# Optimization experiments

Measured on AMD Instinct MI355X. Metric: run time of the kernel, lower is better.

The kernel has to match this reference:

```python
import jax, jax.numpy as jnp
import numpy as np

R, CH, N, E, C, OUT, ED = 2, 2, 20000, 100000, 256, 256, 16


def setup_inputs() -> dict:
    key = jax.random.key(0)
    ks = jax.random.split(key, 11)
    inv = 1.0 / np.sqrt(C)
    return {
        "x": jax.random.normal(ks[0], (R * CH * N, C), jnp.float32),
        "edge_attr": jax.random.normal(ks[1], (E, ED), jnp.float32),
        "edge_weight": jax.random.uniform(ks[2], (R, CH, E, 1), jnp.float32),
        "lin_W": jax.random.normal(ks[3], (C, C), jnp.float32) * inv,
        "lin_b": jax.random.normal(ks[4], (C,), jnp.float32) * inv,
        "linl_W": jax.random.normal(ks[5], (C, OUT), jnp.float32) * inv,
        "linl_b": jax.random.normal(ks[6], (OUT,), jnp.float32) * inv,
        "linr_W": jax.random.normal(ks[7], (C, OUT), jnp.float32) * inv,
        "bond_W": jax.random.normal(ks[8], (ED, C), jnp.float32) / np.sqrt(ED),
        "bond_b": jax.random.normal(ks[9], (C,), jnp.float32) / np.sqrt(ED),
        "edge_index": jax.random.randint(ks[10], (2, E), 0, N, jnp.int64),
    }


def reference(x, edge_attr, edge_weight, lin_W, lin_b, linl_W, linl_b, linr_W,
              bond_W, bond_b, edge_index):
    # bond encoder: (E, ED) -> (E, C), broadcasts as (1, 1, E, C)
    edge_emb = edge_attr @ bond_W + bond_b
    x_l = x @ lin_W + lin_b                      # (R*CH*N, C)
    ux = x_l.reshape(R, CH, N, C)
    src = edge_index[0]
    dst = edge_index[1]
    # gather + add + GELU (exact/erf, matching torch F.gelu) + weight
    msg = jax.nn.gelu(ux[:, :, src, :] + edge_emb, approximate=False) * edge_weight  # (R,CH,E,C)
    # scatter_mean over edge targets
    sums = jnp.zeros((R, CH, N, C), x.dtype).at[:, :, dst, :].add(msg)
    cnt = jnp.zeros((N,), x.dtype).at[dst].add(1.0)
    out = sums / jnp.maximum(cnt, 1.0)[None, None, :, None]
    out = out.reshape(-1, C)                     # (R*CH*N, C)
    return out @ linl_W + linl_b + x @ linr_W
```

## Files before the change

kernel.cpp:

```cpp
#include <hip/hip_runtime.h>
#include <math.h>

#define NN 20000
#define EE 100000
#define CC 256
#define EDM 16
#define RC 4
#define MTOT (RC * NN)

typedef __attribute__((ext_vector_type(8))) short short8;
typedef __attribute__((ext_vector_type(4))) float floatx4;

#define LDK 72

__device__ __forceinline__ unsigned short f2bf(float f) {
    union { float f; unsigned u; } v; v.f = f;
    unsigned r = v.u + 0x7FFF + ((v.u >> 16) & 1);
    return (unsigned short)(r >> 16);
}
__device__ __forceinline__ float bf2f(unsigned short h) {
    union { unsigned u; float f; } v; v.u = ((unsigned)h) << 16;
    return v.f;
}

__device__ __forceinline__ float gelu_fast(float v) {
    const float ax = fabsf(v) * 0.70710678118654752f;
    const float t  = __builtin_amdgcn_rcpf(fmaf(0.3275911f, ax, 1.0f));
    const float p  = t * fmaf(t, fmaf(t, fmaf(t, fmaf(t, 1.061405429f,
                                -1.453152027f), 1.421413741f), -0.284496736f),
                              0.254829592f);
    const float e  = __builtin_amdgcn_exp2f(ax * ax * -1.4426950408889634f);
    const float erf_ax = fmaf(-p, e, 1.0f);
    return fmaf(0.5f * fabsf(v), erf_ax, 0.5f * v);
}

__global__ void k_prep_count(const float* __restrict__ lin_W,
                             const float* __restrict__ linl_W,
                             const float* __restrict__ linr_W,
                             unsigned short* __restrict__ linWT,
                             unsigned short* __restrict__ WbT,
                             const int* __restrict__ eidx,
                             int* __restrict__ cnt) {
    const int b = blockIdx.x;
    const int t = threadIdx.x;
    if (b < CC) {
        linWT[b * CC + t]      = f2bf(lin_W[t * CC + b]);
        WbT[b * 512 + t]       = f2bf(linl_W[t * CC + b]);
        WbT[b * 512 + 256 + t] = f2bf(linr_W[t * CC + b]);
    } else {
        int e = (b - CC) * 256 + t;
        if (e < EE) atomicAdd(cnt + eidx[EE + e], 1);
    }
}

template <int KTOT, int OUTBF16, int A1BF16>
__global__ __launch_bounds__(256) void k_mm(const float* __restrict__ A1f,
                                            const unsigned short* __restrict__ A1b,
                                            const float* __restrict__ A2,
                                            const unsigned short* __restrict__ BT,
                                            const float* __restrict__ bias,
                                            float* __restrict__ Cf,
                                            unsigned short* __restrict__ Cb) {
    __shared__ unsigned short As[64 * LDK];
    __shared__ unsigned short Bs[256 * LDK];
    const int tid  = threadIdx.x;
    const int lane = tid & 63;
    const int wave = tid >> 6;
    const int i0   = blockIdx.x * 64;
    const int l15  = lane & 15;
    const int q4   = lane >> 4;

    floatx4 acc[4][4];
#pragma unroll
    for (int mt = 0; mt < 4; mt++)
#pragma unroll
        for (int nt = 0; nt < 4; nt++) acc[mt][nt] = (floatx4)0.0f;

    for (int kc = 0; kc < KTOT; kc += 64) {
        __syncthreads();
        const int first = (kc < 256);
        const int kco   = first ? kc : kc - 256;
#pragma unroll
        for (int it = 0; it < 2; it++) {
            int q = tid + it * 256;
            int r = q >> 3;
            int c = q & 7;
            if (A1BF16 && first) {
                *(uint4*)(As + r * LDK + c * 8) =
                    *(const uint4*)(A1b + (size_t)(i0 + r) * CC + kco + c * 8);
            } else {
                const float* src = (first ? A1f : A2) + (size_t)(i0 + r) * CC + kco + c * 8;
                float4 v0 = *(const float4*)(src);
                float4 v1 = *(const float4*)(src + 4);
                uint4 p;
                p.x = (unsigned)f2bf(v0.x) | ((unsigned)f2bf(v0.y) << 16);
                p.y = (unsigned)f2bf(v0.z) | ((unsigned)f2bf(v0.w) << 16);
                p.z = (unsigned)f2bf(v1.x) | ((unsigned)f2bf(v1.y) << 16);
                p.w = (unsigned)f2bf(v1.z) | ((unsigned)f2bf(v1.w) << 16);
                *(uint4*)(As + r * LDK + c * 8) = p;
            }
        }
#pragma unroll
        for (int it = 0; it < 8; it++) {
            int q = tid + it * 256;
            int n = q >> 3;
            int c = q & 7;
            *(uint4*)(Bs + n * LDK + c * 8) =
                *(const uint4*)(BT + (size_t)n * KTOT + kc + c * 8);
        }
        __syncthreads();
#pragma unroll
        for (int kk = 0; kk < 64; kk += 32) {
            short8 a[4], b[4];
#pragma unroll
            for (int mt = 0; mt < 4; mt++)
                a[mt] = *(const short8*)(As + (mt * 16 + l15) * LDK + kk + q4 * 8);
#pragma unroll
            for (int nt = 0; nt < 4; nt++)
                b[nt] = *(const short8*)(Bs + (wave * 64 + nt * 16 + l15) * LDK + kk + q4 * 8);
#pragma unroll
            for (int mt = 0; mt < 4; mt++)
#pragma unroll
                for (int nt = 0; nt < 4; nt++)
                    acc[mt][nt] = __builtin_amdgcn_mfma_f32_16x16x32_bf16(
                        a[mt], b[nt], acc[mt][nt], 0, 0, 0);
        }
    }
#pragma unroll
    for (int nt = 0; nt < 4; nt++) {
        const int col = wave * 64 + nt * 16 + l15;
        const float bz = bias[col];
#pragma unroll
        for (int mt = 0; mt < 4; mt++) {
#pragma unroll
            for (int r = 0; r < 4; r++) {
                const int row = i0 + mt * 16 + q4 * 4 + r;
                const float v = acc[mt][nt][r] + bz;
                if (OUTBF16) Cb[(size_t)row * CC + col] = f2bf(v);
                else         Cf[(size_t)row * CC + col] = v;
            }
        }
    }
}

#define SCAN_T 1024
#define SCHUNK 20
__global__ __launch_bounds__(1024) void k_scan(const int* __restrict__ cnt,
                                               int* __restrict__ offs,
                                               int* __restrict__ cursor) {
    __shared__ int ps[SCAN_T];
    const int t = threadIdx.x;
    const int base = t * SCHUNK;
    int s = 0;
#pragma unroll
    for (int i = 0; i < SCHUNK; i++) {
        int idx = base + i;
        if (idx < NN) s += cnt[idx];
    }
    ps[t] = s;
    __syncthreads();
    for (int off = 1; off < SCAN_T; off <<= 1) {
        int v = (t >= off) ? ps[t - off] : 0;
        __syncthreads();
        ps[t] += v;
        __syncthreads();
    }
    int excl = (t == 0) ? 0 : ps[t - 1];
#pragma unroll
    for (int i = 0; i < SCHUNK; i++) {
        int idx = base + i;
        if (idx < NN) {
            offs[idx]   = excl;
            cursor[idx] = excl;
            excl += cnt[idx];
        }
    }
    if (t == SCAN_T - 1) offs[NN] = ps[SCAN_T - 1];
}

__global__ void k_scatter(const int* __restrict__ eidx, int* __restrict__ cursor,
                          int* __restrict__ bucket) {
    int e = blockIdx.x * 256 + threadIdx.x;
    if (e < EE) {
        int d = eidx[EE + e];
        int p = atomicAdd(cursor + d, 1);
        bucket[p] = e;
    }
}

template <int MEANBF16>
__global__ __launch_bounds__(256) void k_agg(const unsigned short* __restrict__ xlb,
                                             const float* __restrict__ edge_attr,
                                             const float* __restrict__ ew,
                                             const float* __restrict__ bond_W,
                                             const float* __restrict__ bond_b,
                                             const int* __restrict__ eidx,
                                             const int* __restrict__ offs,
                                             const int* __restrict__ bucket,
                                             float* __restrict__ mean_f,
                                             unsigned short* __restrict__ mean_b) {
    const int n = blockIdx.x;
    const int c = threadIdx.x;
    const int beg = offs[n], end = offs[n + 1];
    const float bb = bond_b[c];
    float bw[EDM];
#pragma unroll
    for (int k = 0; k < EDM; k++) bw[k] = bond_W[k * CC + c];

    float a0 = 0.f, a1 = 0.f, a2 = 0.f, a3 = 0.f;

#pragma unroll 2
    for (int j = beg; j < end; j++) {
        const int e   = __builtin_amdgcn_readfirstlane(bucket[j]);
        const int src = __builtin_amdgcn_readfirstlane(eidx[e]);
        const float w0 = ew[e];
        const float w1 = ew[EE + e];
        const float w2 = ew[2 * EE + e];
        const float w3 = ew[3 * EE + e];
        const float* ea = edge_attr + (size_t)e * EDM;
        float emb = bb;
#pragma unroll
        for (int k = 0; k < EDM; k++)
            emb = fmaf(ea[k], bw[k], emb);
        const size_t sb = (size_t)src * CC + c;
        float v0 = bf2f(xlb[sb])                       + emb;
        float v1 = bf2f(xlb[sb + (size_t)NN * CC])     + emb;
        float v2 = bf2f(xlb[sb + (size_t)2 * NN * CC]) + emb;
        float v3 = bf2f(xlb[sb + (size_t)3 * NN * CC]) + emb;
        a0 += gelu_fast(v0) * w0;
        a1 += gelu_fast(v1) * w1;
        a2 += gelu_fast(v2) * w2;
        a3 += gelu_fast(v3) * w3;
    }
    const float inv = 1.0f / fmaxf((float)(end - beg), 1.0f);
    const size_t ob = (size_t)n * CC + c;
    if (MEANBF16) {
        mean_b[ob]                       = f2bf(a0 * inv);
        mean_b[ob + (size_t)NN * CC]     = f2bf(a1 * inv);
        mean_b[ob + (size_t)2 * NN * CC] = f2bf(a2 * inv);
        mean_b[ob + (size_t)3 * NN * CC] = f2bf(a3 * inv);
    } else {
        mean_f[ob]                       = a0 * inv;
        mean_f[ob + (size_t)NN * CC]     = a1 * inv;
        mean_f[ob + (size_t)2 * NN * CC] = a2 * inv;
        mean_f[ob + (size_t)3 * NN * CC] = a3 * inv;
    }
}

extern "C" void kernel_launch(void* const* d_in, const int* in_sizes, int n_in,
                              void* d_out, int out_size, void* d_ws, size_t ws_size,
                              hipStream_t stream) {
    (void)in_sizes; (void)n_in; (void)out_size;
    const float* x           = (const float*)d_in[0];
    const float* edge_attr   = (const float*)d_in[1];
    const float* edge_weight = (const float*)d_in[2];
    const float* lin_W       = (const float*)d_in[3];
    const float* lin_b       = (const float*)d_in[4];
    const float* linl_W      = (const float*)d_in[5];
    const float* linl_b      = (const float*)d_in[6];
    const float* linr_W      = (const float*)d_in[7];
    const float* bond_W      = (const float*)d_in[8];
    const float* bond_b      = (const float*)d_in[9];
    const int*   edge_index  = (const int*)d_in[10];

    unsigned short* xlb   = (unsigned short*)d_ws;
    unsigned short* linWT = xlb + (size_t)MTOT * CC;
    unsigned short* WbT   = linWT + CC * CC;
    int* cnt    = (int*)(WbT + CC * 512);
    int* offs   = cnt + NN;
    int* cursor = offs + NN + 1;
    int* bucket = cursor + NN;
    uintptr_t mb_addr = (((uintptr_t)(bucket + EE)) + 255) & ~(uintptr_t)255;
    unsigned short* mean_b = (unsigned short*)mb_addr;
    const size_t need = (mb_addr - (uintptr_t)d_ws) + (size_t)MTOT * CC * 2;
    const int use_bf16 = (ws_size >= need);

    hipMemsetAsync(cnt, 0, NN * sizeof(int), stream);

    k_prep_count<<<CC + (EE + 255) / 256, 256, 0, stream>>>(
        lin_W, linl_W, linr_W, linWT, WbT, edge_index, cnt);
    k_mm<256, 1, 0><<<MTOT / 64, 256, 0, stream>>>(x, nullptr, x, linWT, lin_b,
                                                   nullptr, xlb);
    k_scan<<<1, SCAN_T, 0, stream>>>(cnt, offs, cursor);
    k_scatter<<<(EE + 255) / 256, 256, 0, stream>>>(edge_index, cursor, bucket);

    if (use_bf16) {
        k_agg<1><<<NN, 256, 0, stream>>>(xlb, edge_attr, edge_weight, bond_W, bond_b,
                                         edge_index, offs, bucket, nullptr, mean_b);
        k_mm<512, 0, 1><<<MTOT / 64, 256, 0, stream>>>(nullptr, mean_b, x, WbT, linl_b,
                                                       (float*)d_out, nullptr);
    } else {
        float* mean = (float*)d_out;
        k_agg<0><<<NN, 256, 0, stream>>>(xlb, edge_attr, edge_weight, bond_W, bond_b,
                                         edge_index, offs, bucket, mean, nullptr);
        k_mm<512, 0, 0><<<MTOT / 64, 256, 0, stream>>>(mean, nullptr, x, WbT, linl_b,
                                                       (float*)d_out, nullptr);
    }
}
```

Measured before the change: 398.2 us.

## Retile GEMMs to 128x128 blocks with direct global-to-LDS loads

Replaces the 64-row by 256-column GEMM tile with a 128x128 tile on a 2D grid, using a 2x2 wave layout. The bf16 operands are loaded with global_load_lds straight into LDS, which skips the register staging. The LDS row padding is dropped and the fp32 mean fallback path is removed, so the kernel always uses the bf16 mean buffer. Explicit readfirstlane in the aggregation loop is also removed. The goal is better operand reuse per block and lower load overhead, but the unpadded LDS layout may cause bank conflicts on the fragment reads.

```diff
diff --git a/kernel.cpp b/kernel.cpp
--- a/kernel.cpp
+++ b/kernel.cpp
@@ -10,8 +10,6 @@
 
 typedef __attribute__((ext_vector_type(8))) short short8;
 typedef __attribute__((ext_vector_type(4))) float floatx4;
-
-#define LDK 72
 
 __device__ __forceinline__ unsigned short f2bf(float f) {
     union { float f; unsigned u; } v; v.f = f;
@@ -33,6 +31,11 @@
     const float erf_ax = fmaf(-p, e, 1.0f);
     return fmaf(0.5f * fabsf(v), erf_ax, 0.5f * v);
 }
+
+#define GLDS16(gp, lp)                                                        \
+    __builtin_amdgcn_global_load_lds(                                         \
+        (const __attribute__((address_space(1))) unsigned int*)(gp),          \
+        (__attribute__((address_space(3))) unsigned int*)(lp), 16, 0, 0)
 
 __global__ void k_prep_count(const float* __restrict__ lin_W,
                              const float* __restrict__ linl_W,
@@ -54,21 +57,26 @@
 }
 
 template <int KTOT, int OUTBF16, int A1BF16>
-__global__ __launch_bounds__(256) void k_mm(const float* __restrict__ A1f,
-                                            const unsigned short* __restrict__ A1b,
-                                            const float* __restrict__ A2,
-                                            const unsigned short* __restrict__ BT,
-                                            const float* __restrict__ bias,
-                                            float* __restrict__ Cf,
-                                            unsigned short* __restrict__ Cb) {
-    __shared__ unsigned short As[64 * LDK];
-    __shared__ unsigned short Bs[256 * LDK];
+__global__ __launch_bounds__(256) void k_mmb(const float* __restrict__ A1f,
+                                             const unsigned short* __restrict__ A1b,
+                                             const float* __restrict__ A2f,
+                                             const unsigned short* __restrict__ BT,
+                                             const float* __restrict__ bias,
+                                             float* __restrict__ Cf,
+                                             unsigned short* __restrict__ Cb) {
+    __shared__ unsigned short As[128 * 64];
+    __shared__ unsigned short Bs[128 * 64];
     const int tid  = threadIdx.x;
     const int lane = tid & 63;
     const int wave = tid >> 6;
-    const int i0   = blockIdx.x * 64;
+    const int wr   = wave >> 1;
+    const int wc   = wave & 1;
     const int l15  = lane & 15;
     const int q4   = lane >> 4;
+    const int lr8  = lane >> 3;
+    const int lc8  = lane & 7;
+    const int i0   = blockIdx.x * 128;
+    const int n0   = blockIdx.y * 128;
 
     floatx4 acc[4][4];
 #pragma unroll
@@ -81,32 +89,37 @@
         const int first = (kc < 256);
         const int kco   = first ? kc : kc - 256;
 #pragma unroll
-        for (int it = 0; it < 2; it++) {
-            int q = tid + it * 256;
-            int r = q >> 3;
-            int c = q & 7;
-            if (A1BF16 && first) {
-                *(uint4*)(As + r * LDK + c * 8) =
-                    *(const uint4*)(A1b + (size_t)(i0 + r) * CC + kco + c * 8);
-            } else {
-                const float* src = (first ? A1f : A2) + (size_t)(i0 + r) * CC + kco + c * 8;
-                float4 v0 = *(const float4*)(src);
-                float4 v1 = *(const float4*)(src + 4);
+        for (int it = 0; it < 4; it++) {
+            const int op = wave * 4 + it;
+            const unsigned short* g =
+                BT + (size_t)(n0 + op * 8 + lr8) * KTOT + kc + lc8 * 8;
+            GLDS16(g, Bs + op * 512);
+        }
+        if (A1BF16 && first) {
+#pragma unroll
+            for (int it = 0; it < 4; it++) {
+                const int op = wave * 4 + it;
+                const unsigned short* g =
+                    A1b + (size_t)(i0 + op * 8 + lr8) * CC + kc + lc8 * 8;
+                GLDS16(g, As + op * 512);
+            }
+        } else {
+            const float* af = first ? A1f : A2f;
+#pragma unroll
+            for (int w = 0; w < 4; w++) {
+                const int q  = w * 256 + tid;
+                const int r  = q >> 3;
+                const int c8 = q & 7;
+                const float* s = af + (size_t)(i0 + r) * CC + kco + c8 * 8;
+                float4 v0 = *(const float4*)(s);
+                float4 v1 = *(const float4*)(s + 4);
                 uint4 p;
                 p.x = (unsigned)f2bf(v0.x) | ((unsigned)f2bf(v0.y) << 16);
                 p.y = (unsigned)f2bf(v0.z) | ((unsigned)f2bf(v0.w) << 16);
                 p.z = (unsigned)f2bf(v1.x) | ((unsigned)f2bf(v1.y) << 16);
                 p.w = (unsigned)f2bf(v1.z) | ((unsigned)f2bf(v1.w) << 16);
-                *(uint4*)(As + r * LDK + c * 8) = p;
+                *(uint4*)(As + r * 64 + c8 * 8) = p;
             }
-        }
-#pragma unroll
-        for (int it = 0; it < 8; it++) {
-            int q = tid + it * 256;
-            int n = q >> 3;
-            int c = q & 7;
-            *(uint4*)(Bs + n * LDK + c * 8) =
-                *(const uint4*)(BT + (size_t)n * KTOT + kc + c * 8);
         }
         __syncthreads();
 #pragma unroll
@@ -114,10 +127,10 @@
             short8 a[4], b[4];
 #pragma unroll
             for (int mt = 0; mt < 4; mt++)
-                a[mt] = *(const short8*)(As + (mt * 16 + l15) * LDK + kk + q4 * 8);
+                a[mt] = *(const short8*)(As + (wr * 64 + mt * 16 + l15) * 64 + kk + q4 * 8);
 #pragma unroll
             for (int nt = 0; nt < 4; nt++)
-                b[nt] = *(const short8*)(Bs + (wave * 64 + nt * 16 + l15) * LDK + kk + q4 * 8);
+                b[nt] = *(const short8*)(Bs + (wc * 64 + nt * 16 + l15) * 64 + kk + q4 * 8);
 #pragma unroll
             for (int mt = 0; mt < 4; mt++)
 #pragma unroll
@@ -128,13 +141,13 @@
     }
 #pragma unroll
     for (int nt = 0; nt < 4; nt++) {
-        const int col = wave * 64 + nt * 16 + l15;
+        const int col = n0 + wc * 64 + nt * 16 + l15;
         const float bz = bias[col];
 #pragma unroll
         for (int mt = 0; mt < 4; mt++) {
 #pragma unroll
             for (int r = 0; r < 4; r++) {
-                const int row = i0 + mt * 16 + q4 * 4 + r;
+                const int row = i0 + wr * 64 + mt * 16 + q4 * 4 + r;
                 const float v = acc[mt][nt][r] + bz;
                 if (OUTBF16) Cb[(size_t)row * CC + col] = f2bf(v);
                 else         Cf[(size_t)row * CC + col] = v;
@@ -188,7 +201,6 @@
     }
 }
 
-template <int MEANBF16>
 __global__ __launch_bounds__(256) void k_agg(const unsigned short* __restrict__ xlb,
                                              const float* __restrict__ edge_attr,
                                              const float* __restrict__ ew,
@@ -197,7 +209,6 @@
                                              const int* __restrict__ eidx,
                                              const int* __restrict__ offs,
                                              const int* __restrict__ bucket,
-                                             float* __restrict__ mean_f,
                                              unsigned short* __restrict__ mean_b) {
     const int n = blockIdx.x;
     const int c = threadIdx.x;
@@ -211,8 +222,8 @@
 
 #pragma unroll 2
     for (int j = beg; j < end; j++) {
-        const int e   = __builtin_amdgcn_readfirstlane(bucket[j]);
-        const int src = __builtin_amdgcn_readfirstlane(eidx[e]);
+        const int e   = bucket[j];
+        const int src = eidx[e];
         const float w0 = ew[e];
         const float w1 = ew[EE + e];
         const float w2 = ew[2 * EE + e];
@@ -234,23 +245,16 @@
     }
     const float inv = 1.0f / fmaxf((float)(end - beg), 1.0f);
     const size_t ob = (size_t)n * CC + c;
-    if (MEANBF16) {
-        mean_b[ob]                       = f2bf(a0 * inv);
-        mean_b[ob + (size_t)NN * CC]     = f2bf(a1 * inv);
-        mean_b[ob + (size_t)2 * NN * CC] = f2bf(a2 * inv);
-        mean_b[ob + (size_t)3 * NN * CC] = f2bf(a3 * inv);
-    } else {
-        mean_f[ob]                       = a0 * inv;
-        mean_f[ob + (size_t)NN * CC]     = a1 * inv;
-        mean_f[ob + (size_t)2 * NN * CC] = a2 * inv;
-        mean_f[ob + (size_t)3 * NN * CC] = a3 * inv;
-    }
+    mean_b[ob]                       = f2bf(a0 * inv);
+    mean_b[ob + (size_t)NN * CC]     = f2bf(a1 * inv);
+    mean_b[ob + (size_t)2 * NN * CC] = f2bf(a2 * inv);
+    mean_b[ob + (size_t)3 * NN * CC] = f2bf(a3 * inv);
 }
 
 extern "C" void kernel_launch(void* const* d_in, const int* in_sizes, int n_in,
                               void* d_out, int out_size, void* d_ws, size_t ws_size,
                               hipStream_t stream) {
-    (void)in_sizes; (void)n_in; (void)out_size;
+    (void)in_sizes; (void)n_in; (void)out_size; (void)ws_size;
     const float* x           = (const float*)d_in[0];
     const float* edge_attr   = (const float*)d_in[1];
     const float* edge_weight = (const float*)d_in[2];
@@ -272,28 +276,17 @@
     int* bucket = cursor + NN;
     uintptr_t mb_addr = (((uintptr_t)(bucket + EE)) + 255) & ~(uintptr_t)255;
     unsigned short* mean_b = (unsigned short*)mb_addr;
-    const size_t need = (mb_addr - (uintptr_t)d_ws) + (size_t)MTOT * CC * 2;
-    const int use_bf16 = (ws_size >= need);
 
     hipMemsetAsync(cnt, 0, NN * sizeof(int), stream);
 
     k_prep_count<<<CC + (EE + 255) / 256, 256, 0, stream>>>(
         lin_W, linl_W, linr_W, linWT, WbT, edge_index, cnt);
-    k_mm<256, 1, 0><<<MTOT / 64, 256, 0, stream>>>(x, nullptr, x, linWT, lin_b,
-                                                   nullptr, xlb);
+    k_mmb<256, 1, 0><<<dim3(MTOT / 128, 2), 256, 0, stream>>>(
+        x, nullptr, nullptr, linWT, lin_b, nullptr, xlb);
     k_scan<<<1, SCAN_T, 0, stream>>>(cnt, offs, cursor);
     k_scatter<<<(EE + 255) / 256, 256, 0, stream>>>(edge_index, cursor, bucket);
-
-    if (use_bf16) {
-        k_agg<1><<<NN, 256, 0, stream>>>(xlb, edge_attr, edge_weight, bond_W, bond_b,
-                                         edge_index, offs, bucket, nullptr, mean_b);
-        k_mm<512, 0, 1><<<MTOT / 64, 256, 0, stream>>>(nullptr, mean_b, x, WbT, linl_b,
-                                                       (float*)d_out, nullptr);
-    } else {
-        float* mean = (float*)d_out;
-        k_agg<0><<<NN, 256, 0, stream>>>(xlb, edge_attr, edge_weight, bond_W, bond_b,
-                                         edge_index, offs, bucket, mean, nullptr);
-        k_mm<512, 0, 0><<<MTOT / 64, 256, 0, stream>>>(mean, nullptr, x, WbT, linl_b,
-                                                       (float*)d_out, nullptr);
-    }
-}
+    k_agg<<<NN, 256, 0, stream>>>(xlb, edge_attr, edge_weight, bond_W, bond_b,
+                                  edge_index, offs, bucket, mean_b);
+    k_mmb<512, 0, 1><<<dim3(MTOT / 128, 2), 256, 0, stream>>>(
+        nullptr, mean_b, x, WbT, linl_b, (float*)d_out, nullptr);
+}
```

Result: faster. 372.5 us (-6.5%).
